# Performance work log

Hardware: AMD Instinct MI355X
Metric: run time of the kernel (lower is better)

The kernel has to match this reference:

```python
import jax, jax.numpy as jnp
import numpy as np

DIM = 1024
NUM_HEADS = 16
SCALE = DIM ** (-0.5)  # NOTE: source scales by full dim, not head_dim


def setup_inputs() -> dict:
    key = jax.random.key(0)
    ks = jax.random.split(key, 10)
    B, N, C = 2, 2048, DIM
    s = 0.02
    return {
        "x": jax.random.normal(ks[0], (B, N, C), dtype=jnp.float32),
        "queries": jax.random.normal(ks[1], (B, N, C), dtype=jnp.float32),
        "wq": jax.random.normal(ks[2], (C, C), dtype=jnp.float32) * s,
        "bq": jnp.zeros((C,), dtype=jnp.float32),
        "wk": jax.random.normal(ks[3], (C, C), dtype=jnp.float32) * s,
        "bk": jnp.zeros((C,), dtype=jnp.float32),
        "wv": jax.random.normal(ks[4], (C, C), dtype=jnp.float32) * s,
        "bv": jnp.zeros((C,), dtype=jnp.float32),
        "wo": jax.random.normal(ks[5], (C, C), dtype=jnp.float32) * s,
        "bo": jnp.zeros((C,), dtype=jnp.float32),
    }


def reference(x, queries, wq, bq, wk, bk, wv, bv, wo, bo):
    B, N, C = queries.shape
    H = NUM_HEADS
    D = C // H
    # torch Linear: y = x @ W.T + b  (W is [out, in])
    q = (queries @ wq.T + bq).reshape(B, N, H, D).transpose(0, 2, 1, 3)  # [B,H,N,D]
    k = (x @ wk.T + bk).reshape(B, N, H, D).transpose(0, 2, 1, 3)
    v = (x @ wv.T + bv).reshape(B, N, H, D).transpose(0, 2, 1, 3)
    attn = jnp.einsum("bhqd,bhkd->bhqk", q, k) * SCALE  # full-dim scale per source
    attn = jax.nn.softmax(attn, axis=-1)
    out = jnp.einsum("bhqk,bhkd->bhqd", attn, v)  # [B,H,N,D]
    out = out.transpose(0, 2, 1, 3).reshape(B, N, C)
    return out @ wo.T + bo
```

## Files before the change

kernel.cpp:

```cpp
#include <hip/hip_runtime.h>
#include <hip/hip_bf16.h>

typedef __attribute__((ext_vector_type(8))) short bf16x8;
typedef __attribute__((ext_vector_type(4))) float f32x4;
typedef unsigned short u16;
typedef unsigned int u32;

#define MFMA16(a,b,c) __builtin_amdgcn_mfma_f32_16x16x32_bf16((a),(b),(c),0,0,0)

#if defined(__has_builtin) && __has_builtin(__builtin_amdgcn_exp2f)
#define EXP2(x) __builtin_amdgcn_exp2f(x)
#else
#define EXP2(x) exp2f(x)
#endif

#define QSCALE 0.045084220027780106f

__device__ __forceinline__ u16 f2bf(float f) {
  union { float f; unsigned int u; } v; v.f = f;
  unsigned int r = v.u + 0x7FFFu + ((v.u >> 16) & 1u);
  return (u16)(r >> 16);
}

__device__ __forceinline__ u32 pkbf(float a, float b) {
  union { __hip_bfloat162 h; u32 u; } cv;
  cv.h = __float22bfloat162_rn(make_float2(a, b));
  return cv.u;
}

__device__ __forceinline__ void gld16(const void* g, void* l) {
  __builtin_amdgcn_global_load_lds(
      (__attribute__((address_space(1))) void*)(g),
      (__attribute__((address_space(3))) void*)(l), 16, 0, 0);
}

__global__ __launch_bounds__(256) void cast_all(
    const float* __restrict__ x, const float* __restrict__ qu,
    const float* __restrict__ wq, const float* __restrict__ wk,
    const float* __restrict__ wv, const float* __restrict__ wo,
    u16* __restrict__ xb, u16* __restrict__ qub,
    u16* __restrict__ wqb, u16* __restrict__ wkb,
    u16* __restrict__ wvb, u16* __restrict__ wob)
{
  int i = blockIdx.x * 256 + threadIdx.x;
  const float4* src; u16* dst; int off;
  if (i < 1048576)      { src = (const float4*)qu; dst = qub; off = i; }
  else if (i < 2097152) { src = (const float4*)x;  dst = xb;  off = i - 1048576; }
  else if (i < 2359296) { src = (const float4*)wq; dst = wqb; off = i - 2097152; }
  else if (i < 2621440) { src = (const float4*)wk; dst = wkb; off = i - 2359296; }
  else if (i < 2883584) { src = (const float4*)wv; dst = wvb; off = i - 2621440; }
  else                  { src = (const float4*)wo; dst = wob; off = i - 2883584; }
  float4 v = src[off];
  ushort4 r; r.x = f2bf(v.x); r.y = f2bf(v.y); r.z = f2bf(v.z); r.w = f2bf(v.w);
  ((ushort4*)dst)[off] = r;
}

__global__ __launch_bounds__(256) void gemm_qkv(
    const u16* __restrict__ qub, const u16* __restrict__ xb,
    const u16* __restrict__ wqb, const u16* __restrict__ wkb, const u16* __restrict__ wvb,
    const float* __restrict__ bq, const float* __restrict__ bk, const float* __restrict__ bv,
    u16* __restrict__ qhd, u16* __restrict__ khd, u16* __restrict__ vtd)
{
  __shared__ u16 As[128 * 64];
  __shared__ u16 Bs[128 * 64];
  int tid = threadIdx.x, w = tid >> 6, lane = tid & 63;
  int bm = blockIdx.x, bn = blockIdx.y, z = blockIdx.z;
  int wm = w >> 1, wn = w & 1;
  const u16* A = (z == 0) ? qub : xb;
  const u16* W = (z == 0) ? wqb : (z == 1) ? wkb : wvb;
  f32x4 acc[4][4] = {};
  for (int k0 = 0; k0 < 1024; k0 += 64) {
#pragma unroll
    for (int i = 0; i < 4; i++) {
      int seg = i * 256 + w * 64 + lane;
      int row = seg >> 3, pseg = seg & 7;
      int lseg = pseg ^ (row & 7);
      gld16(A + (size_t)(bm * 128 + row) * 1024 + k0 + lseg * 8,
            &As[(i * 256 + w * 64) * 8]);
      gld16(W + (size_t)(bn * 128 + row) * 1024 + k0 + lseg * 8,
            &Bs[(i * 256 + w * 64) * 8]);
    }
    __syncthreads();
#pragma unroll
    for (int ks = 0; ks < 2; ks++) {
      bf16x8 af[4], bfr[4];
#pragma unroll
      for (int mt = 0; mt < 4; mt++) {
        int row = wm * 64 + mt * 16 + (lane & 15);
        int cseg = (ks * 4 + (lane >> 4)) ^ (row & 7);
        af[mt] = *(const bf16x8*)&As[(row * 8 + cseg) * 8];
      }
#pragma unroll
      for (int nt = 0; nt < 4; nt++) {
        int row = wn * 64 + nt * 16 + (lane & 15);
        int cseg = (ks * 4 + (lane >> 4)) ^ (row & 7);
        bfr[nt] = *(const bf16x8*)&Bs[(row * 8 + cseg) * 8];
      }
#pragma unroll
      for (int mt = 0; mt < 4; mt++)
#pragma unroll
        for (int nt = 0; nt < 4; nt++)
          acc[mt][nt] = MFMA16(af[mt], bfr[nt], acc[mt][nt]);
    }
    __syncthreads();
  }
  const float* bias = (z == 0) ? bq : (z == 1) ? bk : bv;
  u16* dst = (z == 0) ? qhd : khd;
#pragma unroll
  for (int nt = 0; nt < 4; nt++) {
    int o = bn * 128 + wn * 64 + nt * 16 + (lane & 15);
    float bval = bias[o];
    int h = o >> 6, d = o & 63;
#pragma unroll
    for (int mt = 0; mt < 4; mt++)
#pragma unroll
      for (int j = 0; j < 4; j++) {
        int m = bm * 128 + wm * 64 + mt * 16 + (lane >> 4) * 4 + j;
        int b = m >> 11, n = m & 2047;
        float val = acc[mt][nt][j] + bval;
        if (z == 0)
          dst[((size_t)(b * 16 + h) * 2048 + n) * 64 + d] = f2bf(val * QSCALE);
        else if (z == 1)
          dst[((size_t)(b * 16 + h) * 2048 + n) * 64 + d] = f2bf(val);
        else {
          int np = (n & ~63) | ((n & 15) << 2) | ((n >> 4) & 3);
          vtd[((size_t)(b * 16 + h) * 64 + d) * 2048 + np] = f2bf(val);
        }
      }
  }
}

__global__ __launch_bounds__(256, 2) void attn(
    const u16* __restrict__ qh, const u16* __restrict__ kh,
    const u16* __restrict__ vt, u16* __restrict__ ot)
{
  __shared__ u16 Pb[4][64 * 72];
  __shared__ u16 Qs[64 * 72];
  __shared__ float Ls[4][64];
  int tid = threadIdx.x, w = tid >> 6, lane = tid & 63;
  int c = lane & 15, quad = lane >> 4;
  int qt = blockIdx.x, bh = blockIdx.y;
  const u16* qp = qh + ((size_t)bh * 2048 + qt * 64) * 64;
  const u16* kp = kh + ((size_t)bh * 2048 + w * 512) * 64;
  const u16* vp = vt + (size_t)bh * 64 * 2048;

  {
    int row = tid >> 2, ch = tid & 3;
    *(bf16x8*)&Qs[row * 72 + ch * 16]     = *(const bf16x8*)(qp + row * 64 + ch * 16);
    *(bf16x8*)&Qs[row * 72 + ch * 16 + 8] = *(const bf16x8*)(qp + row * 64 + ch * 16 + 8);
  }
  bf16x8 Kf[4][2];
#pragma unroll
  for (int nt = 0; nt < 4; nt++)
#pragma unroll
    for (int ks = 0; ks < 2; ks++)
      Kf[nt][ks] = *(const bf16x8*)(kp + (size_t)(nt * 16 + c) * 64 + ks * 32 + quad * 8);
  __syncthreads();

  f32x4 O[4] = {};
  f32x4 ls[4] = {};
  bf16x8 Vf[4][2];
  for (int it = 0; it < 8; it++) {
#pragma unroll
    for (int b = 0; b < 4; b++)
#pragma unroll
      for (int ks2 = 0; ks2 < 2; ks2++)
        Vf[b][ks2] = *(const bf16x8*)(vp + (size_t)(w * 16 + c) * 2048 +
                                      (b * 8 + it) * 64 + ks2 * 32 + quad * 8);
#pragma unroll
    for (int mt = 0; mt < 4; mt++) {
      bf16x8 q0 = *(const bf16x8*)&Qs[(mt * 16 + c) * 72 + quad * 8];
      bf16x8 q1 = *(const bf16x8*)&Qs[(mt * 16 + c) * 72 + 32 + quad * 8];
      f32x4 S0 = {}, S1 = {}, S2 = {}, S3 = {};
      S0 = MFMA16(q0, Kf[0][0], S0); S0 = MFMA16(q1, Kf[0][1], S0);
      S1 = MFMA16(q0, Kf[1][0], S1); S1 = MFMA16(q1, Kf[1][1], S1);
      S2 = MFMA16(q0, Kf[2][0], S2); S2 = MFMA16(q1, Kf[2][1], S2);
      S3 = MFMA16(q0, Kf[3][0], S3); S3 = MFMA16(q1, Kf[3][1], S3);
#pragma unroll
      for (int j = 0; j < 4; j++) {
        float p0 = EXP2(S0[j]), p1 = EXP2(S1[j]);
        float p2 = EXP2(S2[j]), p3 = EXP2(S3[j]);
        ls[mt][j] += (p0 + p1) + (p2 + p3);
        uint2 pk; pk.x = pkbf(p0, p1); pk.y = pkbf(p2, p3);
        *(uint2*)&Pb[w][(mt * 16 + quad * 4 + j) * 72 + c * 4] = pk;
      }
    }
    if (it < 7) {
#pragma unroll
      for (int nt = 0; nt < 4; nt++)
#pragma unroll
        for (int ks = 0; ks < 2; ks++)
          Kf[nt][ks] = *(const bf16x8*)(kp + (size_t)((it + 1) * 64 + nt * 16 + c) * 64 +
                                        ks * 32 + quad * 8);
    }
    __syncthreads();
#pragma unroll
    for (int b = 0; b < 4; b++)
#pragma unroll
      for (int ks2 = 0; ks2 < 2; ks2++) {
#pragma unroll
        for (int mt = 0; mt < 4; mt++) {
          bf16x8 pa = *(const bf16x8*)&Pb[b][(mt * 16 + c) * 72 + ks2 * 32 + quad * 8];
          O[mt] = MFMA16(pa, Vf[b][ks2], O[mt]);
        }
      }
    __syncthreads();
  }
#pragma unroll
  for (int mt = 0; mt < 4; mt++)
#pragma unroll
    for (int j = 0; j < 4; j++) {
      float s = ls[mt][j];
      s += __shfl_xor(s, 1); s += __shfl_xor(s, 2);
      s += __shfl_xor(s, 4); s += __shfl_xor(s, 8);
      if (c == 0) Ls[w][mt * 16 + quad * 4 + j] = s;
    }
  __syncthreads();
  int b_ = bh >> 4, h = bh & 15;
#pragma unroll
  for (int mt = 0; mt < 4; mt++)
#pragma unroll
    for (int j = 0; j < 4; j++) {
      int q = mt * 16 + quad * 4 + j;
      float inv = 1.0f / (Ls[0][q] + Ls[1][q] + Ls[2][q] + Ls[3][q]);
      int n = qt * 64 + q;
      ot[(((size_t)b_ * 2048 + n) * 16 + h) * 64 + w * 16 + c] = f2bf(O[mt][j] * inv);
    }
}

__global__ __launch_bounds__(256) void gemm_out(
    const u16* __restrict__ Aot, const u16* __restrict__ wob,
    const float* __restrict__ bo, float* __restrict__ out)
{
  __shared__ u16 As[64 * 64];
  __shared__ u16 Bs[128 * 64];
  int tid = threadIdx.x, w = tid >> 6, lane = tid & 63;
  int bm = blockIdx.x, bn = blockIdx.y;
  int wm = w >> 1, wn = w & 1;
  f32x4 acc[2][4] = {};
  for (int k0 = 0; k0 < 1024; k0 += 64) {
#pragma unroll
    for (int i = 0; i < 2; i++) {
      int seg = i * 256 + tid;
      int row = seg >> 3, pseg = seg & 7;
      int lseg = pseg ^ (row & 7);
      gld16(Aot + (size_t)(bm * 64 + row) * 1024 + k0 + lseg * 8,
            &As[(i * 256 + tid - (tid & 7)) * 8 + (tid & 7) * 8]);
    }
#pragma unroll
    for (int i = 0; i < 4; i++) {
      int seg = i * 256 + tid;
      int row = seg >> 3, pseg = seg & 7;
      int lseg = pseg ^ (row & 7);
      gld16(wob + (size_t)(bn * 128 + row) * 1024 + k0 + lseg * 8,
            &Bs[(i * 256 + tid - (tid & 7)) * 8 + (tid & 7) * 8]);
    }
    __syncthreads();
#pragma unroll
    for (int ks = 0; ks < 2; ks++) {
      bf16x8 af[2], bfr[4];
#pragma unroll
      for (int mt = 0; mt < 2; mt++) {
        int row = wm * 32 + mt * 16 + (lane & 15);
        int cseg = (ks * 4 + (lane >> 4)) ^ (row & 7);
        af[mt] = *(const bf16x8*)&As[(row * 8 + cseg) * 8];
      }
#pragma unroll
      for (int nt = 0; nt < 4; nt++) {
        int row = wn * 64 + nt * 16 + (lane & 15);
        int cseg = (ks * 4 + (lane >> 4)) ^ (row & 7);
        bfr[nt] = *(const bf16x8*)&Bs[(row * 8 + cseg) * 8];
      }
#pragma unroll
      for (int mt = 0; mt < 2; mt++)
#pragma unroll
        for (int nt = 0; nt < 4; nt++)
          acc[mt][nt] = MFMA16(af[mt], bfr[nt], acc[mt][nt]);
    }
    __syncthreads();
  }
#pragma unroll
  for (int nt = 0; nt < 4; nt++) {
    int o = bn * 128 + wn * 64 + nt * 16 + (lane & 15);
    float bval = bo[o];
#pragma unroll
    for (int mt = 0; mt < 2; mt++)
#pragma unroll
      for (int j = 0; j < 4; j++) {
        int m = bm * 64 + wm * 32 + mt * 16 + (lane >> 4) * 4 + j;
        out[(size_t)m * 1024 + o] = acc[mt][nt][j] + bval;
      }
  }
}

extern "C" void kernel_launch(void* const* d_in, const int* in_sizes, int n_in,
                              void* d_out, int out_size, void* d_ws, size_t ws_size,
                              hipStream_t stream)
{
  const float* x  = (const float*)d_in[0];
  const float* qu = (const float*)d_in[1];
  const float* wq = (const float*)d_in[2];
  const float* bq = (const float*)d_in[3];
  const float* wk = (const float*)d_in[4];
  const float* bk = (const float*)d_in[5];
  const float* wv = (const float*)d_in[6];
  const float* bv = (const float*)d_in[7];
  const float* wo = (const float*)d_in[8];
  const float* bo = (const float*)d_in[9];
  float* out = (float*)d_out;
  char* ws = (char*)d_ws;
  u16* xb  = (u16*)(ws + (size_t)0);
  u16* qub = (u16*)(ws + ((size_t)8  << 20));
  u16* wqb = (u16*)(ws + ((size_t)16 << 20));
  u16* wkb = (u16*)(ws + ((size_t)18 << 20));
  u16* wvb = (u16*)(ws + ((size_t)20 << 20));
  u16* wob = (u16*)(ws + ((size_t)22 << 20));
  u16* qhd = (u16*)(ws + ((size_t)24 << 20));
  u16* khd = (u16*)(ws + ((size_t)32 << 20));
  u16* vtd = (u16*)(ws + ((size_t)40 << 20));
  u16* otd = (u16*)(ws + ((size_t)48 << 20));

  cast_all<<<12288, 256, 0, stream>>>(x, qu, wq, wk, wv, wo,
                                      xb, qub, wqb, wkb, wvb, wob);
  gemm_qkv<<<dim3(32, 8, 3), 256, 0, stream>>>(qub, xb, wqb, wkb, wvb,
                                               bq, bk, bv, qhd, khd, vtd);
  attn<<<dim3(32, 32), 256, 0, stream>>>(qhd, khd, vtd, otd);
  gemm_out<<<dim3(64, 8), 256, 0, stream>>>(otd, wob, bo, out);
}
```

Before: 239.9 us.

## Split attention keys per wave with private P buffers and LDS reduction

The attention kernel now gives each wave its own 512-key range and computes the full 64x64 output for that range, so the P buffer is private to the wave and the per-iteration block barriers go away. Partial outputs and row sums are reduced across waves through LDS at the end, Q is held in registers, and K is double-buffered with a ping-pong pattern. The V-projection epilogue is transposed through LDS so stores become 16-byte vectors instead of scattered 2-byte writes. In exchange the kernel uses more accumulator registers (O grows to 4x4), drops the 2-blocks-per-CU launch bound, adds an end-of-kernel reduction, and switches EXP2 to plain exp2f.

```diff
diff --git a/kernel.cpp b/kernel.cpp
--- a/kernel.cpp
+++ b/kernel.cpp
@@ -8,11 +8,7 @@
 
 #define MFMA16(a,b,c) __builtin_amdgcn_mfma_f32_16x16x32_bf16((a),(b),(c),0,0,0)
 
-#if defined(__has_builtin) && __has_builtin(__builtin_amdgcn_exp2f)
-#define EXP2(x) __builtin_amdgcn_exp2f(x)
-#else
 #define EXP2(x) exp2f(x)
-#endif
 
 #define QSCALE 0.045084220027780106f
 
@@ -61,9 +57,11 @@
     const float* __restrict__ bq, const float* __restrict__ bk, const float* __restrict__ bv,
     u16* __restrict__ qhd, u16* __restrict__ khd, u16* __restrict__ vtd)
 {
-  __shared__ u16 As[128 * 64];
-  __shared__ u16 Bs[128 * 64];
+  __shared__ u16 sm2[2 * 128 * 64];
+  u16* As = sm2;
+  u16* Bs = sm2 + 128 * 64;
   int tid = threadIdx.x, w = tid >> 6, lane = tid & 63;
+  int c = lane & 15, quad = lane >> 4;
   int bm = blockIdx.x, bn = blockIdx.y, z = blockIdx.z;
   int wm = w >> 1, wn = w & 1;
   const u16* A = (z == 0) ? qub : xb;
@@ -86,14 +84,14 @@
       bf16x8 af[4], bfr[4];
 #pragma unroll
       for (int mt = 0; mt < 4; mt++) {
-        int row = wm * 64 + mt * 16 + (lane & 15);
-        int cseg = (ks * 4 + (lane >> 4)) ^ (row & 7);
+        int row = wm * 64 + mt * 16 + c;
+        int cseg = (ks * 4 + quad) ^ (row & 7);
         af[mt] = *(const bf16x8*)&As[(row * 8 + cseg) * 8];
       }
 #pragma unroll
       for (int nt = 0; nt < 4; nt++) {
-        int row = wn * 64 + nt * 16 + (lane & 15);
-        int cseg = (ks * 4 + (lane >> 4)) ^ (row & 7);
+        int row = wn * 64 + nt * 16 + c;
+        int cseg = (ks * 4 + quad) ^ (row & 7);
         bfr[nt] = *(const bf16x8*)&Bs[(row * 8 + cseg) * 8];
       }
 #pragma unroll
@@ -104,128 +102,194 @@
     }
     __syncthreads();
   }
-  const float* bias = (z == 0) ? bq : (z == 1) ? bk : bv;
-  u16* dst = (z == 0) ? qhd : khd;
-#pragma unroll
-  for (int nt = 0; nt < 4; nt++) {
-    int o = bn * 128 + wn * 64 + nt * 16 + (lane & 15);
-    float bval = bias[o];
-    int h = o >> 6, d = o & 63;
-#pragma unroll
-    for (int mt = 0; mt < 4; mt++)
-#pragma unroll
-      for (int j = 0; j < 4; j++) {
-        int m = bm * 128 + wm * 64 + mt * 16 + (lane >> 4) * 4 + j;
-        int b = m >> 11, n = m & 2047;
-        float val = acc[mt][nt][j] + bval;
-        if (z == 0)
-          dst[((size_t)(b * 16 + h) * 2048 + n) * 64 + d] = f2bf(val * QSCALE);
-        else if (z == 1)
-          dst[((size_t)(b * 16 + h) * 2048 + n) * 64 + d] = f2bf(val);
-        else {
-          int np = (n & ~63) | ((n & 15) << 2) | ((n >> 4) & 3);
-          vtd[((size_t)(b * 16 + h) * 64 + d) * 2048 + np] = f2bf(val);
+  if (z < 2) {
+    const float* bias = (z == 0) ? bq : bk;
+    u16* dst = (z == 0) ? qhd : khd;
+#pragma unroll
+    for (int nt = 0; nt < 4; nt++) {
+      int o = bn * 128 + wn * 64 + nt * 16 + c;
+      float bval = bias[o];
+      int h = o >> 6, d = o & 63;
+#pragma unroll
+      for (int mt = 0; mt < 4; mt++)
+#pragma unroll
+        for (int j = 0; j < 4; j++) {
+          int m = bm * 128 + wm * 64 + mt * 16 + quad * 4 + j;
+          int b = m >> 11, n = m & 2047;
+          float val = acc[mt][nt][j] + bval;
+          if (z == 0)
+            dst[((size_t)(b * 16 + h) * 2048 + n) * 64 + d] = f2bf(val * QSCALE);
+          else
+            dst[((size_t)(b * 16 + h) * 2048 + n) * 64 + d] = f2bf(val);
         }
-      }
-  }
-}
-
-__global__ __launch_bounds__(256, 2) void attn(
+    }
+  } else {
+    u16* LT = sm2;
+    for (int h2 = 0; h2 < 2; h2++) {
+      if (wm == h2) {
+#pragma unroll
+        for (int nt = 0; nt < 4; nt++) {
+          int o = bn * 128 + wn * 64 + nt * 16 + c;
+          float bval = bv[o];
+          int col = wn * 64 + nt * 16 + c;
+#pragma unroll
+          for (int mt = 0; mt < 4; mt++)
+#pragma unroll
+            for (int j = 0; j < 4; j++) {
+              int rl = mt * 16 + quad * 4 + j;
+              LT[rl * 137 + col] = f2bf(acc[mt][nt][j] + bval);
+            }
+        }
+      }
+      __syncthreads();
+      int m0 = bm * 128 + h2 * 64;
+      int b = m0 >> 11, n0 = m0 & 2047;
+      int tk0 = (tid & 7) * 8;
+#pragma unroll
+      for (int pass = 0; pass < 4; pass++) {
+        int cl = pass * 32 + (tid >> 3);
+        int o = bn * 128 + cl, hh = o >> 6, dd = o & 63;
+        u16 tmp[8];
+#pragma unroll
+        for (int i = 0; i < 8; i++) tmp[i] = LT[(tk0 + i) * 137 + cl];
+        uint4 pk4;
+        pk4.x = ((u32)tmp[1] << 16) | tmp[0];
+        pk4.y = ((u32)tmp[3] << 16) | tmp[2];
+        pk4.z = ((u32)tmp[5] << 16) | tmp[4];
+        pk4.w = ((u32)tmp[7] << 16) | tmp[6];
+        *(uint4*)(vtd + ((size_t)(b * 16 + hh) * 64 + dd) * 2048 + n0 + tk0) = pk4;
+      }
+      __syncthreads();
+    }
+  }
+}
+
+__global__ __launch_bounds__(256) void attn(
     const u16* __restrict__ qh, const u16* __restrict__ kh,
     const u16* __restrict__ vt, u16* __restrict__ ot)
 {
-  __shared__ u16 Pb[4][64 * 72];
-  __shared__ u16 Qs[64 * 72];
+  __shared__ __align__(16) char smraw[4 * 64 * 72 * 2];
   __shared__ float Ls[4][64];
   int tid = threadIdx.x, w = tid >> 6, lane = tid & 63;
   int c = lane & 15, quad = lane >> 4;
   int qt = blockIdx.x, bh = blockIdx.y;
   const u16* qp = qh + ((size_t)bh * 2048 + qt * 64) * 64;
   const u16* kp = kh + ((size_t)bh * 2048 + w * 512) * 64;
-  const u16* vp = vt + (size_t)bh * 64 * 2048;
-
-  {
-    int row = tid >> 2, ch = tid & 3;
-    *(bf16x8*)&Qs[row * 72 + ch * 16]     = *(const bf16x8*)(qp + row * 64 + ch * 16);
-    *(bf16x8*)&Qs[row * 72 + ch * 16 + 8] = *(const bf16x8*)(qp + row * 64 + ch * 16 + 8);
-  }
-  bf16x8 Kf[4][2];
+  const u16* vp = vt + (size_t)bh * 64 * 2048 + w * 512;
+  u16* Pw = (u16*)smraw + w * (64 * 72);
+
+  bf16x8 aq[4][2];
+#pragma unroll
+  for (int mt = 0; mt < 4; mt++)
+#pragma unroll
+    for (int ks = 0; ks < 2; ks++)
+      aq[mt][ks] = *(const bf16x8*)(qp + (size_t)(mt * 16 + c) * 64 + ks * 32 + quad * 8);
+
+  bf16x8 Ka[4][2], Kb[4][2];
 #pragma unroll
   for (int nt = 0; nt < 4; nt++)
 #pragma unroll
     for (int ks = 0; ks < 2; ks++)
-      Kf[nt][ks] = *(const bf16x8*)(kp + (size_t)(nt * 16 + c) * 64 + ks * 32 + quad * 8);
+      Ka[nt][ks] = *(const bf16x8*)(kp + (size_t)(nt * 16 + c) * 64 + ks * 32 + quad * 8);
+
+  f32x4 O[4][4] = {};
+  float ls[4] = {0.f, 0.f, 0.f, 0.f};
+
+#define ATTN_STEP(IT, KC, KN)                                                   \
+  {                                                                             \
+    bf16x8 Vf[4][2];                                                            \
+    _Pragma("unroll") for (int dt = 0; dt < 4; dt++)                            \
+      _Pragma("unroll") for (int k2 = 0; k2 < 2; k2++)                          \
+        Vf[dt][k2] = *(const bf16x8*)(vp + (size_t)(dt * 16 + c) * 2048 +       \
+                                      (IT) * 64 + k2 * 32 + quad * 8);          \
+    _Pragma("unroll") for (int mt = 0; mt < 4; mt++) {                          \
+      f32x4 S0 = {}, S1 = {}, S2 = {}, S3 = {};                                 \
+      S0 = MFMA16(KC[0][0], aq[mt][0], S0); S0 = MFMA16(KC[0][1], aq[mt][1], S0); \
+      S1 = MFMA16(KC[1][0], aq[mt][0], S1); S1 = MFMA16(KC[1][1], aq[mt][1], S1); \
+      S2 = MFMA16(KC[2][0], aq[mt][0], S2); S2 = MFMA16(KC[2][1], aq[mt][1], S2); \
+      S3 = MFMA16(KC[3][0], aq[mt][0], S3); S3 = MFMA16(KC[3][1], aq[mt][1], S3); \
+      u16* prow = &Pw[(mt * 16 + c) * 72 + quad * 4];                           \
+      float p0, p1, p2, p3, sacc; uint2 pk;                                     \
+      p0 = EXP2(S0[0]); p1 = EXP2(S0[1]); p2 = EXP2(S0[2]); p3 = EXP2(S0[3]);   \
+      sacc = (p0 + p1) + (p2 + p3);                                             \
+      pk.x = pkbf(p0, p1); pk.y = pkbf(p2, p3); *(uint2*)(prow) = pk;           \
+      p0 = EXP2(S1[0]); p1 = EXP2(S1[1]); p2 = EXP2(S1[2]); p3 = EXP2(S1[3]);   \
+      sacc += (p0 + p1) + (p2 + p3);                                            \
+      pk.x = pkbf(p0, p1); pk.y = pkbf(p2, p3); *(uint2*)(prow + 16) = pk;      \
+      p0 = EXP2(S2[0]); p1 = EXP2(S2[1]); p2 = EXP2(S2[2]); p3 = EXP2(S2[3]);   \
+      sacc += (p0 + p1) + (p2 + p3);                                            \
+      pk.x = pkbf(p0, p1); pk.y = pkbf(p2, p3); *(uint2*)(prow + 32) = pk;      \
+      p0 = EXP2(S3[0]); p1 = EXP2(S3[1]); p2 = EXP2(S3[2]); p3 = EXP2(S3[3]);   \
+      sacc += (p0 + p1) + (p2 + p3);                                            \
+      pk.x = pkbf(p0, p1); pk.y = pkbf(p2, p3); *(uint2*)(prow + 48) = pk;      \
+      ls[mt] += sacc;                                                           \
+    }                                                                           \
+    if ((IT) < 7) {                                                             \
+      _Pragma("unroll") for (int nt = 0; nt < 4; nt++)                          \
+        _Pragma("unroll") for (int ks = 0; ks < 2; ks++)                        \
+          KN[nt][ks] = *(const bf16x8*)(kp +                                    \
+              (size_t)(((IT) + 1) * 64 + nt * 16 + c) * 64 + ks * 32 + quad * 8); \
+    }                                                                           \
+    _Pragma("unroll") for (int mt = 0; mt < 4; mt++)                            \
+      _Pragma("unroll") for (int k2 = 0; k2 < 2; k2++) {                        \
+        bf16x8 pa = *(const bf16x8*)&Pw[(mt * 16 + c) * 72 + k2 * 32 + quad * 8]; \
+        _Pragma("unroll") for (int dt = 0; dt < 4; dt++)                        \
+          O[mt][dt] = MFMA16(pa, Vf[dt][k2], O[mt][dt]);                        \
+      }                                                                         \
+  }
+
+  for (int ii = 0; ii < 4; ii++) {
+    ATTN_STEP(2 * ii,     Ka, Kb)
+    ATTN_STEP(2 * ii + 1, Kb, Ka)
+  }
+#undef ATTN_STEP
+
+#pragma unroll
+  for (int mt = 0; mt < 4; mt++) {
+    float s = ls[mt];
+    s += __shfl_xor(s, 16);
+    s += __shfl_xor(s, 32);
+    ls[mt] = s;
+  }
   __syncthreads();
-
-  f32x4 O[4] = {};
-  f32x4 ls[4] = {};
-  bf16x8 Vf[4][2];
-  for (int it = 0; it < 8; it++) {
-#pragma unroll
-    for (int b = 0; b < 4; b++)
-#pragma unroll
-      for (int ks2 = 0; ks2 < 2; ks2++)
-        Vf[b][ks2] = *(const bf16x8*)(vp + (size_t)(w * 16 + c) * 2048 +
-                                      (b * 8 + it) * 64 + ks2 * 32 + quad * 8);
-#pragma unroll
-    for (int mt = 0; mt < 4; mt++) {
-      bf16x8 q0 = *(const bf16x8*)&Qs[(mt * 16 + c) * 72 + quad * 8];
-      bf16x8 q1 = *(const bf16x8*)&Qs[(mt * 16 + c) * 72 + 32 + quad * 8];
-      f32x4 S0 = {}, S1 = {}, S2 = {}, S3 = {};
-      S0 = MFMA16(q0, Kf[0][0], S0); S0 = MFMA16(q1, Kf[0][1], S0);
-      S1 = MFMA16(q0, Kf[1][0], S1); S1 = MFMA16(q1, Kf[1][1], S1);
-      S2 = MFMA16(q0, Kf[2][0], S2); S2 = MFMA16(q1, Kf[2][1], S2);
-      S3 = MFMA16(q0, Kf[3][0], S3); S3 = MFMA16(q1, Kf[3][1], S3);
-#pragma unroll
-      for (int j = 0; j < 4; j++) {
-        float p0 = EXP2(S0[j]), p1 = EXP2(S1[j]);
-        float p2 = EXP2(S2[j]), p3 = EXP2(S3[j]);
-        ls[mt][j] += (p0 + p1) + (p2 + p3);
-        uint2 pk; pk.x = pkbf(p0, p1); pk.y = pkbf(p2, p3);
-        *(uint2*)&Pb[w][(mt * 16 + quad * 4 + j) * 72 + c * 4] = pk;
-      }
-    }
-    if (it < 7) {
-#pragma unroll
-      for (int nt = 0; nt < 4; nt++)
-#pragma unroll
-        for (int ks = 0; ks < 2; ks++)
-          Kf[nt][ks] = *(const bf16x8*)(kp + (size_t)((it + 1) * 64 + nt * 16 + c) * 64 +
-                                        ks * 32 + quad * 8);
-    }
-    __syncthreads();
-#pragma unroll
-    for (int b = 0; b < 4; b++)
-#pragma unroll
-      for (int ks2 = 0; ks2 < 2; ks2++) {
-#pragma unroll
-        for (int mt = 0; mt < 4; mt++) {
-          bf16x8 pa = *(const bf16x8*)&Pb[b][(mt * 16 + c) * 72 + ks2 * 32 + quad * 8];
-          O[mt] = MFMA16(pa, Vf[b][ks2], O[mt]);
-        }
-      }
-    __syncthreads();
-  }
-#pragma unroll
-  for (int mt = 0; mt < 4; mt++)
-#pragma unroll
-    for (int j = 0; j < 4; j++) {
-      float s = ls[mt][j];
-      s += __shfl_xor(s, 1); s += __shfl_xor(s, 2);
-      s += __shfl_xor(s, 4); s += __shfl_xor(s, 8);
-      if (c == 0) Ls[w][mt * 16 + quad * 4 + j] = s;
-    }
-  __syncthreads();
+  if (lane < 16) {
+#pragma unroll
+    for (int mt = 0; mt < 4; mt++) Ls[w][mt * 16 + c] = ls[mt];
+  }
+  float* Ored = (float*)smraw;
+  float* Ow = Ored + w * (32 * 68);
   int b_ = bh >> 4, h = bh & 15;
-#pragma unroll
-  for (int mt = 0; mt < 4; mt++)
-#pragma unroll
-    for (int j = 0; j < 4; j++) {
-      int q = mt * 16 + quad * 4 + j;
-      float inv = 1.0f / (Ls[0][q] + Ls[1][q] + Ls[2][q] + Ls[3][q]);
-      int n = qt * 64 + q;
-      ot[(((size_t)b_ * 2048 + n) * 16 + h) * 64 + w * 16 + c] = f2bf(O[mt][j] * inv);
-    }
+  for (int r = 0; r < 2; r++) {
+#pragma unroll
+    for (int mh = 0; mh < 2; mh++) {
+      int mt = r * 2 + mh;
+#pragma unroll
+      for (int dt = 0; dt < 4; dt++)
+#pragma unroll
+        for (int j = 0; j < 4; j++)
+          Ow[(mh * 16 + quad * 4 + j) * 68 + dt * 16 + c] = O[mt][dt][j];
+    }
+    __syncthreads();
+    {
+      int qb = tid >> 3, d0 = (tid & 7) * 8;
+      f32x4 sa = {}, sb = {};
+#pragma unroll
+      for (int ww = 0; ww < 4; ww++) {
+        const float* src = Ored + ww * (32 * 68) + qb * 68 + d0;
+        sa += *(const f32x4*)src;
+        sb += *(const f32x4*)(src + 4);
+      }
+      int q64 = r * 32 + qb;
+      float linv = 1.0f / (Ls[0][q64] + Ls[1][q64] + Ls[2][q64] + Ls[3][q64]);
+      uint4 pk4;
+      pk4.x = pkbf(sa[0] * linv, sa[1] * linv);
+      pk4.y = pkbf(sa[2] * linv, sa[3] * linv);
+      pk4.z = pkbf(sb[0] * linv, sb[1] * linv);
+      pk4.w = pkbf(sb[2] * linv, sb[3] * linv);
+      *(uint4*)(ot + (((size_t)b_ * 2048 + qt * 64 + q64) * 16 + h) * 64 + d0) = pk4;
+    }
+    __syncthreads();
+  }
 }
 
 __global__ __launch_bounds__(256) void gemm_out(
```

After: 263.2 us. +9.7%, slower.
